# Kernel tuning notes

Measured on AMD Instinct MI355X. Metric: run time of the kernel, lower is better.

Reference implementation:

```python
import jax, jax.numpy as jnp
import numpy as np

N, K, F, H = 10000, 32, 128, 256  # nodes, max_neighbors, edge_feat_dim, hidden_size
EPS = 1e-5


def layer_norm(x, g, b):
    m = jnp.mean(x, axis=-1, keepdims=True)
    v = jnp.mean(jnp.square(x - m), axis=-1, keepdims=True)
    return (x - m) * jax.lax.rsqrt(v + EPS) * g + b


def setup_inputs() -> dict:
    key = jax.random.key(0)
    ks = jax.random.split(key, 8)
    edge_features = jax.random.normal(ks[0], (N, K, F), dtype=jnp.float32)
    neighbor_mask = jax.random.randint(ks[1], (N, K), 0, 2) > 0
    s_lin = 1.0 / np.sqrt(F)
    s_h = 1.0 / np.sqrt(H)
    return {
        "edge_features": edge_features,
        "neighbor_mask": neighbor_mask,
        "W_lin": jax.random.normal(ks[2], (F, H), dtype=jnp.float32) * s_lin,
        "b_lin": jnp.zeros((H,), dtype=jnp.float32),
        "g_pre": jnp.ones((H,), dtype=jnp.float32),
        "b_pre": jnp.zeros((H,), dtype=jnp.float32),
        "W_ff1": jax.random.normal(ks[3], (H, H), dtype=jnp.float32) * s_h,
        "b_ff1": jnp.zeros((H,), dtype=jnp.float32),
        "W_ff2": jax.random.normal(ks[4], (H, H), dtype=jnp.float32) * s_h,
        "b_ff2": jnp.zeros((H,), dtype=jnp.float32),
        "g_node": jnp.ones((H,), dtype=jnp.float32),
        "b_node": jnp.zeros((H,), dtype=jnp.float32),
        "g_edge": jnp.ones((H,), dtype=jnp.float32),
        "b_edge": jnp.zeros((H,), dtype=jnp.float32),
    }


def reference(edge_features, neighbor_mask, W_lin, b_lin, g_pre, b_pre,
              W_ff1, b_ff1, W_ff2, b_ff2, g_node, b_node, g_edge, b_edge):
    # edge linear: [N,K,F] @ [F,H] -> [N,K,H]
    edge_hidden = jnp.einsum("nkf,fh->nkh", edge_features, W_lin) + b_lin
    # pre-norm FFN with residual
    h = layer_norm(edge_hidden, g_pre, b_pre)
    h = jax.nn.gelu(jnp.einsum("nkh,hd->nkd", h, W_ff1) + b_ff1)
    h = jnp.einsum("nkd,dh->nkh", h, W_ff2) + b_ff2
    edge_output = edge_hidden + h
    # masked neighbor aggregation (segment-style reduce over padded neighbors)
    node_output = jnp.sum(
        jnp.where(neighbor_mask[:, :, None], edge_output, 0.0), axis=1)
    # output normalization on both node and edge features
    node_out = layer_norm(node_output, g_node, b_node)
    edge_out = layer_norm(edge_output, g_edge, b_edge)
    return (node_out, edge_out)
```

## Files before the change

### kernel.cpp

```cpp
#include <hip/hip_runtime.h>

typedef float f32x4 __attribute__((ext_vector_type(4)));
typedef float f32x2 __attribute__((ext_vector_type(2)));
typedef short bf16x8 __attribute__((ext_vector_type(8)));
typedef unsigned int u32;
typedef unsigned int u32x2 __attribute__((ext_vector_type(2)));
typedef unsigned short u16;

#define DEVI static __device__ __forceinline__

static constexpr int MROWS = 320000;
static constexpr int HD    = 256;
static constexpr int NNODE = 10000;

DEVI u16 f2bf(float f) {
  u32 u = __builtin_bit_cast(u32, f);
  u = (u + 0x7fffu + ((u >> 16) & 1u)) >> 16;
  return (u16)u;
}
DEVI float bf2f(u16 s) {
  u32 u = ((u32)s) << 16;
  return __builtin_bit_cast(float, u);
}
DEVI float gelu_f(float y) {
  float z = 0.7978845608028654f * (y + 0.044715f * y * y * y);
  float E = __expf(2.f * z);
  return y * (1.f - 1.f / (E + 1.f));
}

__global__ void prep_weights(const float* __restrict__ W_lin, const float* __restrict__ g_pre,
                             const float* __restrict__ W_ff1, const float* __restrict__ W_ff2,
                             u16* __restrict__ Wlt, u16* __restrict__ W1gt, u16* __restrict__ W2t)
{
  int e = blockIdx.x * 256 + threadIdx.x;
  if (e < 32768) {
    int c = e >> 7, k = e & 127;
    Wlt[e] = f2bf(W_lin[k * 256 + c]);
  } else if (e < 32768 + 65536) {
    int e2 = e - 32768; int c = e2 >> 8, k = e2 & 255;
    W1gt[e2] = f2bf(g_pre[k] * W_ff1[k * 256 + c]);
  } else if (e < 163840) {
    int e3 = e - 98304; int c = e3 >> 8, k = e3 & 255;
    W2t[e3] = f2bf(W_ff2[k * 256 + c]);
  }
}

__global__ void prep_uv(const float* __restrict__ W_ff1, const float* __restrict__ g_pre,
                        const float* __restrict__ b_pre, const float* __restrict__ b_ff1,
                        float* __restrict__ u, float* __restrict__ v)
{
  int c = threadIdx.x;
  float uu = 0.f, vv = 0.f;
  for (int k = 0; k < 256; ++k) {
    float w = W_ff1[k * 256 + c];
    uu += g_pre[k] * w;
    vv += b_pre[k] * w;
  }
  u[c] = uu;
  v[c] = vv + b_ff1[c];
}

DEVI void stage_w(const u16* __restrict__ Wt, int KD2, int c, char* buf, int wid, int lane) {
#pragma unroll
  for (int j2 = 0; j2 < 2; ++j2) {
    int j = wid * 2 + j2;
    int L = j * 1024 + lane * 16;
    int cL = L >> 6;
    int kk = ((L >> 4) & 3) ^ ((cL >> 1) & 3);
    const char* g = (const char*)Wt + (size_t)cL * (size_t)KD2 + (size_t)c * 64 + (size_t)kk * 16;
    __builtin_amdgcn_global_load_lds((const __attribute__((address_space(1))) void*)g,
                                     (__attribute__((address_space(3))) void*)(buf + j * 1024),
                                     16, 0, 0);
  }
}

template<int NK, int STRIDE, bool SKIP0>
DEVI void run_gemm(f32x4 (&acc)[4][4], const char* xbase, const u16* __restrict__ Wt,
                   char* wstBase, int wid, int lane, int wr, int wc)
{
  const int lo = lane & 15, hi = lane >> 4;
  constexpr int KD2 = NK * 64;
  if (!SKIP0) stage_w(Wt, KD2, 0, wstBase, wid, lane);
  __syncthreads();
#pragma unroll
  for (int c = 0; c < NK; ++c) {
    if (c + 1 < NK) stage_w(Wt, KD2, c + 1, wstBase + ((c + 1) & 1) * 16384, wid, lane);
    bf16x8 a[4], b[4];
#pragma unroll
    for (int rg = 0; rg < 4; ++rg) {
      int r = wr * 64 + rg * 16 + lo;
      a[rg] = *(const bf16x8*)(xbase + r * STRIDE + ((((c * 4 + hi) ^ (r & 7))) << 4));
    }
    const char* wb = wstBase + (c & 1) * 16384;
#pragma unroll
    for (int nt = 0; nt < 4; ++nt) {
      int cc = wc * 64 + nt * 16 + lo;
      b[nt] = *(const bf16x8*)(wb + cc * 64 + ((hi ^ ((cc >> 1) & 3)) << 4));
    }
#pragma unroll
    for (int nt = 0; nt < 4; ++nt)
#pragma unroll
      for (int rg = 0; rg < 4; ++rg)
        acc[rg][nt] = __builtin_amdgcn_mfma_f32_16x16x32_bf16(b[nt], a[rg], acc[rg][nt], 0, 0, 0);
    __syncthreads();
  }
}

__global__ __launch_bounds__(512, 2)
void mega_kernel(const float* __restrict__ EF, const int* __restrict__ nmask,
                 const u16* __restrict__ Wlt, const u16* __restrict__ W1gt, const u16* __restrict__ W2t,
                 const float* __restrict__ b_lin, const float* __restrict__ uc, const float* __restrict__ vc,
                 const float* __restrict__ b_ff2, const float* __restrict__ g_edge, const float* __restrict__ b_edge,
                 const float* __restrict__ g_node, const float* __restrict__ b_node,
                 float* __restrict__ node_out, float* __restrict__ edge_out)
{
  const int tid  = threadIdx.x;
  const int wid  = tid >> 6;
  const int lane = tid & 63;
  const int lo   = lane & 15;
  const int hi   = lane >> 4;
  const int wr   = wid >> 2;
  const int wc   = wid & 3;
  const int tile0 = blockIdx.x * 128;

  __shared__ char  xLDS[65536];
  __shared__ char  wst[2][16384];
  __shared__ float part[4][128][2];
  __shared__ float red[8][2];

  stage_w(Wlt, 256, 0, &wst[0][0], wid, lane);
#pragma unroll
  for (int it = 0; it < 4; ++it) {
    int ch = tid + it * 512;
    int r = ch >> 4, sl = ch & 15;
    const float* src = EF + (size_t)(tile0 + r) * 128 + sl * 8;
    f32x4 x0 = *(const f32x4*)src;
    f32x4 x1 = *(const f32x4*)(src + 4);
    bf16x8 t;
    t[0] = (short)f2bf(x0[0]); t[1] = (short)f2bf(x0[1]);
    t[2] = (short)f2bf(x0[2]); t[3] = (short)f2bf(x0[3]);
    t[4] = (short)f2bf(x1[0]); t[5] = (short)f2bf(x1[1]);
    t[6] = (short)f2bf(x1[2]); t[7] = (short)f2bf(x1[3]);
    *(bf16x8*)(xLDS + r * 256 + ((sl ^ (r & 7)) << 4)) = t;
  }

  f32x4 acc[4][4];
#pragma unroll
  for (int rg = 0; rg < 4; ++rg)
#pragma unroll
    for (int nt = 0; nt < 4; ++nt) acc[rg][nt] = f32x4{0.f, 0.f, 0.f, 0.f};

  run_gemm<4, 256, true>(acc, xLDS, Wlt, &wst[0][0], wid, lane, wr, wc);

  u32x2 ehreg[4][4];
  {
    f32x4 bl[4];
#pragma unroll
    for (int nt = 0; nt < 4; ++nt)
      bl[nt] = *(const f32x4*)(b_lin + wc * 64 + nt * 16 + hi * 4);
#pragma unroll
    for (int rg = 0; rg < 4; ++rg) {
      int r = wr * 64 + rg * 16 + lo;
      float ss = 0.f, qq = 0.f;
#pragma unroll
      for (int nt = 0; nt < 4; ++nt) {
        f32x4 x = acc[rg][nt] + bl[nt];
        u32 w0 = (u32)f2bf(x[0]) | ((u32)f2bf(x[1]) << 16);
        u32 w1 = (u32)f2bf(x[2]) | ((u32)f2bf(x[3]) << 16);
        ehreg[rg][nt] = u32x2{w0, w1};
        int slot = wc * 8 + nt * 2 + (hi >> 1);
        *(u32x2*)(xLDS + r * 512 + ((slot ^ (r & 7)) << 4) + (hi & 1) * 8) = ehreg[rg][nt];
        ss += x[0] + x[1] + x[2] + x[3];
        qq += x[0]*x[0] + x[1]*x[1] + x[2]*x[2] + x[3]*x[3];
      }
      ss += __shfl_xor(ss, 16); ss += __shfl_xor(ss, 32);
      qq += __shfl_xor(qq, 16); qq += __shfl_xor(qq, 32);
      if (hi == 0) { part[wc][r][0] = ss; part[wc][r][1] = qq; }
    }
  }
  __syncthreads();
  if (tid < 128) {
    float ss = part[0][tid][0] + part[1][tid][0] + part[2][tid][0] + part[3][tid][0];
    float qq = part[0][tid][1] + part[1][tid][1] + part[2][tid][1] + part[3][tid][1];
    float m  = ss * (1.f / 256.f);
    float var = qq * (1.f / 256.f) - m * m;
    part[0][tid][0] = m;
    part[0][tid][1] = rsqrtf(var + 1e-5f);
  }
  __syncthreads();
  float rsr[4], rmr[4];
#pragma unroll
  for (int rg = 0; rg < 4; ++rg) {
    int r = wr * 64 + rg * 16 + lo;
    float m = part[0][r][0], rs = part[0][r][1];
    rsr[rg] = rs; rmr[rg] = m * rs;
  }

#pragma unroll
  for (int rg = 0; rg < 4; ++rg)
#pragma unroll
    for (int nt = 0; nt < 4; ++nt) acc[rg][nt] = f32x4{0.f, 0.f, 0.f, 0.f};
  run_gemm<8, 512, false>(acc, xLDS, W1gt, &wst[0][0], wid, lane, wr, wc);

  {
    f32x4 u4[4], v4[4];
#pragma unroll
    for (int nt = 0; nt < 4; ++nt) {
      u4[nt] = *(const f32x4*)(uc + wc * 64 + nt * 16 + hi * 4);
      v4[nt] = *(const f32x4*)(vc + wc * 64 + nt * 16 + hi * 4);
    }
#pragma unroll
    for (int rg = 0; rg < 4; ++rg) {
      int r = wr * 64 + rg * 16 + lo;
#pragma unroll
      for (int nt = 0; nt < 4; ++nt) {
        f32x4 y = acc[rg][nt] * rsr[rg] - u4[nt] * rmr[rg] + v4[nt];
        u32 w0 = (u32)f2bf(gelu_f(y[0])) | ((u32)f2bf(gelu_f(y[1])) << 16);
        u32 w1 = (u32)f2bf(gelu_f(y[2])) | ((u32)f2bf(gelu_f(y[3])) << 16);
        int slot = wc * 8 + nt * 2 + (hi >> 1);
        *(u32x2*)(xLDS + r * 512 + ((slot ^ (r & 7)) << 4) + (hi & 1) * 8) = u32x2{w0, w1};
      }
    }
  }

#pragma unroll
  for (int rg = 0; rg < 4; ++rg)
#pragma unroll
    for (int nt = 0; nt < 4; ++nt) acc[rg][nt] = f32x4{0.f, 0.f, 0.f, 0.f};
  run_gemm<8, 512, false>(acc, xLDS, W2t, &wst[0][0], wid, lane, wr, wc);

  f32x4 eo[4][4];
  f32x4 ge4[4], be4[4];
  {
    f32x4 b2[4];
#pragma unroll
    for (int nt = 0; nt < 4; ++nt) {
      b2[nt]  = *(const f32x4*)(b_ff2  + wc * 64 + nt * 16 + hi * 4);
      ge4[nt] = *(const f32x4*)(g_edge + wc * 64 + nt * 16 + hi * 4);
      be4[nt] = *(const f32x4*)(b_edge + wc * 64 + nt * 16 + hi * 4);
    }
#pragma unroll
    for (int rg = 0; rg < 4; ++rg) {
      int r = wr * 64 + rg * 16 + lo;
      float ss = 0.f, qq = 0.f;
#pragma unroll
      for (int nt = 0; nt < 4; ++nt) {
        f32x4 x = acc[rg][nt] + b2[nt];
        x[0] += bf2f((u16)(ehreg[rg][nt][0] & 0xffffu));
        x[1] += bf2f((u16)(ehreg[rg][nt][0] >> 16));
        x[2] += bf2f((u16)(ehreg[rg][nt][1] & 0xffffu));
        x[3] += bf2f((u16)(ehreg[rg][nt][1] >> 16));
        eo[rg][nt] = x;
        ss += x[0] + x[1] + x[2] + x[3];
        qq += x[0]*x[0] + x[1]*x[1] + x[2]*x[2] + x[3]*x[3];
      }
      ss += __shfl_xor(ss, 16); ss += __shfl_xor(ss, 32);
      qq += __shfl_xor(qq, 16); qq += __shfl_xor(qq, 32);
      if (hi == 0) { part[wc][r][0] = ss; part[wc][r][1] = qq; }
    }
  }
  __syncthreads();
  if (tid < 128) {
    float ss = part[0][tid][0] + part[1][tid][0] + part[2][tid][0] + part[3][tid][0];
    float qq = part[0][tid][1] + part[1][tid][1] + part[2][tid][1] + part[3][tid][1];
    float m  = ss * (1.f / 256.f);
    float var = qq * (1.f / 256.f) - m * m;
    part[0][tid][0] = m;
    part[0][tid][1] = rsqrtf(var + 1e-5f);
  }
  __syncthreads();
#pragma unroll
  for (int rg = 0; rg < 4; ++rg) {
    int r = wr * 64 + rg * 16 + lo;
    float m2 = part[0][r][0], rs2 = part[0][r][1];
#pragma unroll
    for (int nt = 0; nt < 4; ++nt) {
      f32x4 x = eo[rg][nt];
      u32 w0 = (u32)f2bf(x[0]) | ((u32)f2bf(x[1]) << 16);
      u32 w1 = (u32)f2bf(x[2]) | ((u32)f2bf(x[3]) << 16);
      int slot = wc * 8 + nt * 2 + (hi >> 1);
      *(u32x2*)(xLDS + r * 512 + ((slot ^ (r & 7)) << 4) + (hi & 1) * 8) = u32x2{w0, w1};
      f32x4 o = (x - m2) * rs2 * ge4[nt] + be4[nt];
      *(f32x4*)(edge_out + (size_t)(tile0 + r) * 256 + wc * 64 + nt * 16 + hi * 4) = o;
    }
  }
  __syncthreads();

  float* np = (float*)&wst[0][0];
  {
    int nd = tid >> 7, rest = tid & 127, cc = rest >> 2, rq = rest & 3;
    float p[8] = {0.f,0.f,0.f,0.f,0.f,0.f,0.f,0.f};
#pragma unroll
    for (int j = 0; j < 8; ++j) {
      int r = nd * 32 + rq * 8 + j;
      if (nmask[tile0 + r] != 0) {
        bf16x8 v = *(const bf16x8*)(xLDS + r * 512 + ((cc ^ (r & 7)) << 4));
#pragma unroll
        for (int k = 0; k < 8; ++k) p[k] += bf2f((u16)v[k]);
      }
    }
    int base = ((nd * 32 + cc) * 4 + rq) * 8;
    int sx = cc & 7;
#pragma unroll
    for (int j = 0; j < 8; ++j) np[base + (j ^ sx)] = p[j];
  }
  __syncthreads();

  {
    int nd = tid >> 7, cp = tid & 127;
    int c0 = cp * 2;
    int cc = c0 >> 3, j0 = c0 & 7, sx = cc & 7;
    float s0 = 0.f, s1 = 0.f;
#pragma unroll
    for (int rq = 0; rq < 4; ++rq) {
      int base = ((nd * 32 + cc) * 4 + rq) * 8;
      s0 += np[base + (j0 ^ sx)];
      s1 += np[base + ((j0 + 1) ^ sx)];
    }
    float ss = s0 + s1, qq = s0 * s0 + s1 * s1;
#pragma unroll
    for (int d = 1; d < 64; d <<= 1) { ss += __shfl_xor(ss, d); qq += __shfl_xor(qq, d); }
    if (lane == 0) { red[wid][0] = ss; red[wid][1] = qq; }
    __syncthreads();
    ss = red[nd * 2][0] + red[nd * 2 + 1][0];
    qq = red[nd * 2][1] + red[nd * 2 + 1][1];
    float m  = ss * (1.f / 256.f);
    float var = qq * (1.f / 256.f) - m * m;
    float rs = rsqrtf(var + 1e-5f);
    f32x2 o;
    o[0] = (s0 - m) * rs * g_node[c0]     + b_node[c0];
    o[1] = (s1 - m) * rs * g_node[c0 + 1] + b_node[c0 + 1];
    *(f32x2*)(node_out + (size_t)(blockIdx.x * 4 + nd) * 256 + c0) = o;
  }
}

extern "C" void kernel_launch(void* const* d_in, const int* in_sizes, int n_in,
                              void* d_out, int out_size, void* d_ws, size_t ws_size,
                              hipStream_t stream)
{
  (void)in_sizes; (void)n_in; (void)out_size; (void)ws_size;
  const float* edge_features = (const float*)d_in[0];
  const int*   nmask  = (const int*)d_in[1];
  const float* W_lin  = (const float*)d_in[2];
  const float* b_lin  = (const float*)d_in[3];
  const float* g_pre  = (const float*)d_in[4];
  const float* b_pre  = (const float*)d_in[5];
  const float* W_ff1  = (const float*)d_in[6];
  const float* b_ff1  = (const float*)d_in[7];
  const float* W_ff2  = (const float*)d_in[8];
  const float* b_ff2  = (const float*)d_in[9];
  const float* g_node = (const float*)d_in[10];
  const float* b_node = (const float*)d_in[11];
  const float* g_edge = (const float*)d_in[12];
  const float* b_edge = (const float*)d_in[13];

  char* ws = (char*)d_ws;
  u16* Wlt   = (u16*)ws;   ws += 256 * 128 * 2;
  u16* W1gt  = (u16*)ws;   ws += 256 * 256 * 2;
  u16* W2t   = (u16*)ws;   ws += 256 * 256 * 2;
  float* uc  = (float*)ws; ws += 256 * 4;
  float* vc  = (float*)ws; ws += 256 * 4;

  float* node_out = (float*)d_out;
  float* edge_out = (float*)d_out + (size_t)NNODE * HD;

  prep_weights<<<640, 256, 0, stream>>>(W_lin, g_pre, W_ff1, W_ff2, Wlt, W1gt, W2t);
  prep_uv<<<1, 256, 0, stream>>>(W_ff1, g_pre, b_pre, b_ff1, uc, vc);
  mega_kernel<<<2500, 512, 0, stream>>>(edge_features, nmask, Wlt, W1gt, W2t,
                                        b_lin, uc, vc, b_ff2, g_edge, b_edge,
                                        g_node, b_node, node_out, edge_out);
}
```

Baseline: 701.5 us.

## Halve row tile, read weights directly from global, drop LDS weight staging

```diff
diff --git a/kernel.cpp b/kernel.cpp
--- a/kernel.cpp
+++ b/kernel.cpp
@@ -9,7 +9,6 @@
 
 #define DEVI static __device__ __forceinline__
 
-static constexpr int MROWS = 320000;
 static constexpr int HD    = 256;
 static constexpr int NNODE = 10000;
 
@@ -51,6 +50,7 @@
 {
   int c = threadIdx.x;
   float uu = 0.f, vv = 0.f;
+#pragma unroll 8
   for (int k = 0; k < 256; ++k) {
     float w = W_ff1[k * 256 + c];
     uu += g_pre[k] * w;
@@ -60,53 +60,33 @@
   v[c] = vv + b_ff1[c];
 }
 
-DEVI void stage_w(const u16* __restrict__ Wt, int KD2, int c, char* buf, int wid, int lane) {
-#pragma unroll
-  for (int j2 = 0; j2 < 2; ++j2) {
-    int j = wid * 2 + j2;
-    int L = j * 1024 + lane * 16;
-    int cL = L >> 6;
-    int kk = ((L >> 4) & 3) ^ ((cL >> 1) & 3);
-    const char* g = (const char*)Wt + (size_t)cL * (size_t)KD2 + (size_t)c * 64 + (size_t)kk * 16;
-    __builtin_amdgcn_global_load_lds((const __attribute__((address_space(1))) void*)g,
-                                     (__attribute__((address_space(3))) void*)(buf + j * 1024),
-                                     16, 0, 0);
-  }
-}
-
-template<int NK, int STRIDE, bool SKIP0>
-DEVI void run_gemm(f32x4 (&acc)[4][4], const char* xbase, const u16* __restrict__ Wt,
-                   char* wstBase, int wid, int lane, int wr, int wc)
-{
-  const int lo = lane & 15, hi = lane >> 4;
-  constexpr int KD2 = NK * 64;
-  if (!SKIP0) stage_w(Wt, KD2, 0, wstBase, wid, lane);
-  __syncthreads();
-#pragma unroll
-  for (int c = 0; c < NK; ++c) {
-    if (c + 1 < NK) stage_w(Wt, KD2, c + 1, wstBase + ((c + 1) & 1) * 16384, wid, lane);
+template<int NK, int STRIDE>
+DEVI void run_gemm(f32x4 (&acc)[4][4], const char* __restrict__ xbase,
+                   const u16* __restrict__ Wt, int lo, int hi, int wc)
+{
+  const char* __restrict__ wp = (const char*)Wt;
+#pragma unroll
+  for (int ks = 0; ks < NK; ++ks) {
     bf16x8 a[4], b[4];
-#pragma unroll
-    for (int rg = 0; rg < 4; ++rg) {
-      int r = wr * 64 + rg * 16 + lo;
-      a[rg] = *(const bf16x8*)(xbase + r * STRIDE + ((((c * 4 + hi) ^ (r & 7))) << 4));
-    }
-    const char* wb = wstBase + (c & 1) * 16384;
 #pragma unroll
     for (int nt = 0; nt < 4; ++nt) {
       int cc = wc * 64 + nt * 16 + lo;
-      b[nt] = *(const bf16x8*)(wb + cc * 64 + ((hi ^ ((cc >> 1) & 3)) << 4));
+      b[nt] = *(const bf16x8*)(wp + (size_t)cc * (NK * 64) + ks * 64 + hi * 16);
+    }
+#pragma unroll
+    for (int rg = 0; rg < 4; ++rg) {
+      int r = rg * 16 + lo;
+      a[rg] = *(const bf16x8*)(xbase + r * STRIDE + (((ks * 4 + hi) ^ (r & 7)) << 4));
     }
 #pragma unroll
     for (int nt = 0; nt < 4; ++nt)
 #pragma unroll
       for (int rg = 0; rg < 4; ++rg)
         acc[rg][nt] = __builtin_amdgcn_mfma_f32_16x16x32_bf16(b[nt], a[rg], acc[rg][nt], 0, 0, 0);
-    __syncthreads();
-  }
-}
-
-__global__ __launch_bounds__(512, 2)
+  }
+}
+
+__global__ __launch_bounds__(256, 3)
 void mega_kernel(const float* __restrict__ EF, const int* __restrict__ nmask,
                  const u16* __restrict__ Wlt, const u16* __restrict__ W1gt, const u16* __restrict__ W2t,
                  const float* __restrict__ b_lin, const float* __restrict__ uc, const float* __restrict__ vc,
@@ -115,27 +95,26 @@
                  float* __restrict__ node_out, float* __restrict__ edge_out)
 {
   const int tid  = threadIdx.x;
-  const int wid  = tid >> 6;
   const int lane = tid & 63;
+  const int wc   = tid >> 6;
   const int lo   = lane & 15;
   const int hi   = lane >> 4;
-  const int wr   = wid >> 2;
-  const int wc   = wid & 3;
-  const int tile0 = blockIdx.x * 128;
-
-  __shared__ char  xLDS[65536];
-  __shared__ char  wst[2][16384];
-  __shared__ float part[4][128][2];
-  __shared__ float red[8][2];
-
-  stage_w(Wlt, 256, 0, &wst[0][0], wid, lane);
+  const int tile0 = blockIdx.x * 64;
+
+  __shared__ char  xLDS[32768];
+  __shared__ float part[4][64][2];
+  __shared__ int   lm[64];
+  __shared__ float red[4][2];
+
+  if (tid < 64) lm[tid] = nmask[tile0 + tid];
+
 #pragma unroll
   for (int it = 0; it < 4; ++it) {
-    int ch = tid + it * 512;
-    int r = ch >> 4, sl = ch & 15;
+    int idx = it * 256 + tid;
+    int r = idx >> 4, sl = idx & 15;
     const float* src = EF + (size_t)(tile0 + r) * 128 + sl * 8;
-    f32x4 x0 = *(const f32x4*)src;
-    f32x4 x1 = *(const f32x4*)(src + 4);
+    f32x4 x0 = __builtin_nontemporal_load((const f32x4*)src);
+    f32x4 x1 = __builtin_nontemporal_load((const f32x4*)(src + 4));
     bf16x8 t;
     t[0] = (short)f2bf(x0[0]); t[1] = (short)f2bf(x0[1]);
     t[2] = (short)f2bf(x0[2]); t[3] = (short)f2bf(x0[3]);
@@ -143,6 +122,7 @@
     t[6] = (short)f2bf(x1[2]); t[7] = (short)f2bf(x1[3]);
     *(bf16x8*)(xLDS + r * 256 + ((sl ^ (r & 7)) << 4)) = t;
   }
+  __syncthreads();
 
   f32x4 acc[4][4];
 #pragma unroll
@@ -150,7 +130,7 @@
 #pragma unroll
     for (int nt = 0; nt < 4; ++nt) acc[rg][nt] = f32x4{0.f, 0.f, 0.f, 0.f};
 
-  run_gemm<4, 256, true>(acc, xLDS, Wlt, &wst[0][0], wid, lane, wr, wc);
+  run_gemm<4, 256>(acc, xLDS, Wlt, lo, hi, wc);
 
   u32x2 ehreg[4][4];
   {
@@ -160,7 +140,7 @@
       bl[nt] = *(const f32x4*)(b_lin + wc * 64 + nt * 16 + hi * 4);
 #pragma unroll
     for (int rg = 0; rg < 4; ++rg) {
-      int r = wr * 64 + rg * 16 + lo;
+      int r = rg * 16 + lo;
       float ss = 0.f, qq = 0.f;
 #pragma unroll
       for (int nt = 0; nt < 4; ++nt) {
@@ -168,8 +148,6 @@
         u32 w0 = (u32)f2bf(x[0]) | ((u32)f2bf(x[1]) << 16);
         u32 w1 = (u32)f2bf(x[2]) | ((u32)f2bf(x[3]) << 16);
         ehreg[rg][nt] = u32x2{w0, w1};
-        int slot = wc * 8 + nt * 2 + (hi >> 1);
-        *(u32x2*)(xLDS + r * 512 + ((slot ^ (r & 7)) << 4) + (hi & 1) * 8) = ehreg[rg][nt];
         ss += x[0] + x[1] + x[2] + x[3];
         qq += x[0]*x[0] + x[1]*x[1] + x[2]*x[2] + x[3]*x[3];
       }
@@ -179,7 +157,7 @@
     }
   }
   __syncthreads();
-  if (tid < 128) {
+  if (tid < 64) {
     float ss = part[0][tid][0] + part[1][tid][0] + part[2][tid][0] + part[3][tid][0];
     float qq = part[0][tid][1] + part[1][tid][1] + part[2][tid][1] + part[3][tid][1];
     float m  = ss * (1.f / 256.f);
@@ -187,20 +165,23 @@
     part[0][tid][0] = m;
     part[0][tid][1] = rsqrtf(var + 1e-5f);
   }
-  __syncthreads();
-  float rsr[4], rmr[4];
 #pragma unroll
   for (int rg = 0; rg < 4; ++rg) {
-    int r = wr * 64 + rg * 16 + lo;
-    float m = part[0][r][0], rs = part[0][r][1];
-    rsr[rg] = rs; rmr[rg] = m * rs;
-  }
+    int r = rg * 16 + lo;
+#pragma unroll
+    for (int nt = 0; nt < 4; ++nt) {
+      int slot = wc * 8 + nt * 2 + (hi >> 1);
+      *(u32x2*)(xLDS + r * 512 + ((slot ^ (r & 7)) << 4) + (hi & 1) * 8) = ehreg[rg][nt];
+    }
+  }
+  __syncthreads();
 
 #pragma unroll
   for (int rg = 0; rg < 4; ++rg)
 #pragma unroll
     for (int nt = 0; nt < 4; ++nt) acc[rg][nt] = f32x4{0.f, 0.f, 0.f, 0.f};
-  run_gemm<8, 512, false>(acc, xLDS, W1gt, &wst[0][0], wid, lane, wr, wc);
+  run_gemm<8, 512>(acc, xLDS, W1gt, lo, hi, wc);
+  __syncthreads();
 
   {
     f32x4 u4[4], v4[4];
@@ -211,10 +192,13 @@
     }
 #pragma unroll
     for (int rg = 0; rg < 4; ++rg) {
-      int r = wr * 64 + rg * 16 + lo;
+      int r = rg * 16 + lo;
+      float m  = part[0][r][0];
+      float rs = part[0][r][1];
+      float rm = m * rs;
 #pragma unroll
       for (int nt = 0; nt < 4; ++nt) {
-        f32x4 y = acc[rg][nt] * rsr[rg] - u4[nt] * rmr[rg] + v4[nt];
+        f32x4 y = acc[rg][nt] * rs - u4[nt] * rm + v4[nt];
         u32 w0 = (u32)f2bf(gelu_f(y[0])) | ((u32)f2bf(gelu_f(y[1])) << 16);
         u32 w1 = (u32)f2bf(gelu_f(y[2])) | ((u32)f2bf(gelu_f(y[3])) << 16);
         int slot = wc * 8 + nt * 2 + (hi >> 1);
@@ -222,26 +206,22 @@
       }
     }
   }
+  __syncthreads();
 
 #pragma unroll
   for (int rg = 0; rg < 4; ++rg)
 #pragma unroll
     for (int nt = 0; nt < 4; ++nt) acc[rg][nt] = f32x4{0.f, 0.f, 0.f, 0.f};
-  run_gemm<8, 512, false>(acc, xLDS, W2t, &wst[0][0], wid, lane, wr, wc);
-
-  f32x4 eo[4][4];
-  f32x4 ge4[4], be4[4];
+  run_gemm<8, 512>(acc, xLDS, W2t, lo, hi, wc);
+
   {
     f32x4 b2[4];
 #pragma unroll
-    for (int nt = 0; nt < 4; ++nt) {
-      b2[nt]  = *(const f32x4*)(b_ff2  + wc * 64 + nt * 16 + hi * 4);
-      ge4[nt] = *(const f32x4*)(g_edge + wc * 64 + nt * 16 + hi * 4);
-      be4[nt] = *(const f32x4*)(b_edge + wc * 64 + nt * 16 + hi * 4);
-    }
-#pragma unroll
-    for (int rg = 0; rg < 4; ++rg) {
-      int r = wr * 64 + rg * 16 + lo;
+    for (int nt = 0; nt < 4; ++nt)
+      b2[nt] = *(const f32x4*)(b_ff2 + wc * 64 + nt * 16 + hi * 4);
+#pragma unroll
+    for (int rg = 0; rg < 4; ++rg) {
+      int r = rg * 16 + lo;
       float ss = 0.f, qq = 0.f;
 #pragma unroll
       for (int nt = 0; nt < 4; ++nt) {
@@ -250,7 +230,7 @@
         x[1] += bf2f((u16)(ehreg[rg][nt][0] >> 16));
         x[2] += bf2f((u16)(ehreg[rg][nt][1] & 0xffffu));
         x[3] += bf2f((u16)(ehreg[rg][nt][1] >> 16));
-        eo[rg][nt] = x;
+        acc[rg][nt] = x;
         ss += x[0] + x[1] + x[2] + x[3];
         qq += x[0]*x[0] + x[1]*x[1] + x[2]*x[2] + x[3]*x[3];
       }
@@ -260,7 +240,7 @@
     }
   }
   __syncthreads();
-  if (tid < 128) {
+  if (tid < 64) {
     float ss = part[0][tid][0] + part[1][tid][0] + part[2][tid][0] + part[3][tid][0];
     float qq = part[0][tid][1] + part[1][tid][1] + part[2][tid][1] + part[3][tid][1];
     float m  = ss * (1.f / 256.f);
@@ -269,68 +249,66 @@
     part[0][tid][1] = rsqrtf(var + 1e-5f);
   }
   __syncthreads();
-#pragma unroll
-  for (int rg = 0; rg < 4; ++rg) {
-    int r = wr * 64 + rg * 16 + lo;
-    float m2 = part[0][r][0], rs2 = part[0][r][1];
+
+  {
+    f32x4 ge4[4], be4[4];
 #pragma unroll
     for (int nt = 0; nt < 4; ++nt) {
-      f32x4 x = eo[rg][nt];
-      u32 w0 = (u32)f2bf(x[0]) | ((u32)f2bf(x[1]) << 16);
-      u32 w1 = (u32)f2bf(x[2]) | ((u32)f2bf(x[3]) << 16);
-      int slot = wc * 8 + nt * 2 + (hi >> 1);
-      *(u32x2*)(xLDS + r * 512 + ((slot ^ (r & 7)) << 4) + (hi & 1) * 8) = u32x2{w0, w1};
-      f32x4 o = (x - m2) * rs2 * ge4[nt] + be4[nt];
-      *(f32x4*)(edge_out + (size_t)(tile0 + r) * 256 + wc * 64 + nt * 16 + hi * 4) = o;
-    }
-  }
-  __syncthreads();
-
-  float* np = (float*)&wst[0][0];
-  {
-    int nd = tid >> 7, rest = tid & 127, cc = rest >> 2, rq = rest & 3;
-    float p[8] = {0.f,0.f,0.f,0.f,0.f,0.f,0.f,0.f};
-#pragma unroll
-    for (int j = 0; j < 8; ++j) {
-      int r = nd * 32 + rq * 8 + j;
-      if (nmask[tile0 + r] != 0) {
-        bf16x8 v = *(const bf16x8*)(xLDS + r * 512 + ((cc ^ (r & 7)) << 4));
-#pragma unroll
-        for (int k = 0; k < 8; ++k) p[k] += bf2f((u16)v[k]);
-      }
-    }
-    int base = ((nd * 32 + cc) * 4 + rq) * 8;
-    int sx = cc & 7;
-#pragma unroll
-    for (int j = 0; j < 8; ++j) np[base + (j ^ sx)] = p[j];
-  }
-  __syncthreads();
-
-  {
-    int nd = tid >> 7, cp = tid & 127;
-    int c0 = cp * 2;
-    int cc = c0 >> 3, j0 = c0 & 7, sx = cc & 7;
+      ge4[nt] = *(const f32x4*)(g_edge + wc * 64 + nt * 16 + hi * 4);
+      be4[nt] = *(const f32x4*)(b_edge + wc * 64 + nt * 16 + hi * 4);
+    }
+#pragma unroll
+    for (int rg = 0; rg < 4; ++rg) {
+      int r = rg * 16 + lo;
+      float m2  = part[0][r][0];
+      float rs2 = part[0][r][1];
+#pragma unroll
+      for (int nt = 0; nt < 4; ++nt) {
+        f32x4 x = acc[rg][nt];
+        u32 w0 = (u32)f2bf(x[0]) | ((u32)f2bf(x[1]) << 16);
+        u32 w1 = (u32)f2bf(x[2]) | ((u32)f2bf(x[3]) << 16);
+        int slot = wc * 8 + nt * 2 + (hi >> 1);
+        *(u32x2*)(xLDS + r * 512 + ((slot ^ (r & 7)) << 4) + (hi & 1) * 8) = u32x2{w0, w1};
+        f32x4 o = (x - m2) * rs2 * ge4[nt] + be4[nt];
+        __builtin_nontemporal_store(o,
+            (f32x4*)(edge_out + (size_t)(tile0 + r) * 256 + wc * 64 + nt * 16 + hi * 4));
+      }
+    }
+  }
+  __syncthreads();
+
+  {
+    int nd = tid >> 7;
+    int c0 = (tid & 127) * 2;
+    int chunk = c0 >> 3;
+    int wib = (c0 & 7) * 2;
     float s0 = 0.f, s1 = 0.f;
 #pragma unroll
-    for (int rq = 0; rq < 4; ++rq) {
-      int base = ((nd * 32 + cc) * 4 + rq) * 8;
-      s0 += np[base + (j0 ^ sx)];
-      s1 += np[base + ((j0 + 1) ^ sx)];
+    for (int r32 = 0; r32 < 32; ++r32) {
+      int r = nd * 32 + r32;
+      if (lm[r] != 0) {
+        u32 w = *(const u32*)(xLDS + r * 512 + ((chunk ^ (r & 7)) << 4) + wib);
+        s0 += bf2f((u16)(w & 0xffffu));
+        s1 += bf2f((u16)(w >> 16));
+      }
     }
     float ss = s0 + s1, qq = s0 * s0 + s1 * s1;
 #pragma unroll
     for (int d = 1; d < 64; d <<= 1) { ss += __shfl_xor(ss, d); qq += __shfl_xor(qq, d); }
-    if (lane == 0) { red[wid][0] = ss; red[wid][1] = qq; }
+    if (lane == 0) { red[wc][0] = ss; red[wc][1] = qq; }
     __syncthreads();
     ss = red[nd * 2][0] + red[nd * 2 + 1][0];
     qq = red[nd * 2][1] + red[nd * 2 + 1][1];
-    float m  = ss * (1.f / 256.f);
+    float m   = ss * (1.f / 256.f);
     float var = qq * (1.f / 256.f) - m * m;
-    float rs = rsqrtf(var + 1e-5f);
+    float rs  = rsqrtf(var + 1e-5f);
+    f32x2 gn = *(const f32x2*)(g_node + c0);
+    f32x2 bn = *(const f32x2*)(b_node + c0);
     f32x2 o;
-    o[0] = (s0 - m) * rs * g_node[c0]     + b_node[c0];
-    o[1] = (s1 - m) * rs * g_node[c0 + 1] + b_node[c0 + 1];
-    *(f32x2*)(node_out + (size_t)(blockIdx.x * 4 + nd) * 256 + c0) = o;
+    o[0] = (s0 - m) * rs * gn[0] + bn[0];
+    o[1] = (s1 - m) * rs * gn[1] + bn[1];
+    __builtin_nontemporal_store(o,
+        (f32x2*)(node_out + (size_t)(blockIdx.x * 2 + nd) * 256 + c0));
   }
 }
 
@@ -358,15 +336,15 @@
   u16* Wlt   = (u16*)ws;   ws += 256 * 128 * 2;
   u16* W1gt  = (u16*)ws;   ws += 256 * 256 * 2;
   u16* W2t   = (u16*)ws;   ws += 256 * 256 * 2;
-  float* uc  = (float*)ws; ws += 256 * 4;
-  float* vc  = (float*)ws; ws += 256 * 4;
+  float* ucp = (float*)ws; ws += 256 * 4;
+  float* vcp = (float*)ws; ws += 256 * 4;
 
   float* node_out = (float*)d_out;
   float* edge_out = (float*)d_out + (size_t)NNODE * HD;
 
   prep_weights<<<640, 256, 0, stream>>>(W_lin, g_pre, W_ff1, W_ff2, Wlt, W1gt, W2t);
-  prep_uv<<<1, 256, 0, stream>>>(W_ff1, g_pre, b_pre, b_ff1, uc, vc);
-  mega_kernel<<<2500, 512, 0, stream>>>(edge_features, nmask, Wlt, W1gt, W2t,
-                                        b_lin, uc, vc, b_ff2, g_edge, b_edge,
+  prep_uv<<<1, 256, 0, stream>>>(W_ff1, g_pre, b_pre, b_ff1, ucp, vcp);
+  mega_kernel<<<5000, 256, 0, stream>>>(edge_features, nmask, Wlt, W1gt, W2t,
+                                        b_lin, ucp, vcp, b_ff2, g_edge, b_edge,
                                         g_node, b_node, node_out, edge_out);
 }
```

Measured after the change: 754.9 us. 1.08x slower.
